# Optimization experiments

Measured on AMD Instinct MI355X. Metric: run time of the kernel, lower is better.

The kernel has to match this reference:

```python
import jax, jax.numpy as jnp
import numpy as np

N = 100_000        # nodes
E = 1_600_000      # edges
IN_F = 128         # input_features
HID = 64           # hiddens per head
OUT = 64           # outputs
NHEADS = 8
ALPHA = 0.2        # leaky_relu negative slope


def setup_inputs() -> dict:
    key = jax.random.key(0)
    ks = jax.random.split(key, 8)
    x = jax.random.normal(ks[0], (N, IN_F), jnp.float32)
    edges = jax.random.randint(ks[1], (2, E), 0, N)
    # nn.Linear(input_features, input_features)
    W0 = jax.random.normal(ks[2], (IN_F, IN_F), jnp.float32) / np.sqrt(IN_F).astype(np.float32)
    b0 = jnp.zeros((IN_F,), jnp.float32)
    # per-head SpGAT params: W [in, out], a [2*out]
    W_heads = jax.random.normal(ks[3], (NHEADS, IN_F, HID), jnp.float32) * 0.05
    a_heads = jax.random.normal(ks[4], (NHEADS, 2 * HID), jnp.float32) * 0.05
    W_end = jax.random.normal(ks[5], (NHEADS * HID, OUT), jnp.float32) * 0.05
    a_end = jax.random.normal(ks[6], (2 * OUT,), jnp.float32) * 0.05
    return dict(x=x, edges=edges, W0=W0, b0=b0,
                W_heads=W_heads, a_heads=a_heads, W_end=W_end, a_end=a_end)


def _sp_gat_layer(x, src, dst, W, a, apply_elu):
    """Standard sparse GAT layer (pyGAT SpGraphAttentionLayer).

    score_e = a . [h_src || h_dst];  e = exp(-leaky_relu(score))
    out_i = (sum_{e: src=i} e * h_dst) / (sum_{e: src=i} e)
    """
    n = x.shape[0]
    h = x @ W                      # [N, F]
    F = h.shape[1]
    # a.[h_i||h_j] decomposed into per-node scores to avoid [E, 2F] gather
    s_src = h @ a[:F]              # [N]
    s_dst = h @ a[F:]              # [N]
    score = s_src[src] + s_dst[dst]            # [E]
    edge_e = jnp.exp(-jax.nn.leaky_relu(score, ALPHA))
    rowsum = jax.ops.segment_sum(edge_e, src, num_segments=n)            # [N]
    agg = jax.ops.segment_sum(edge_e[:, None] * h[dst], src, num_segments=n)  # [N, F]
    out = agg / (rowsum[:, None] + 1e-16)
    return jax.nn.elu(out) if apply_elu else out


def reference(x, edges, W0, b0, W_heads, a_heads, W_end, a_end):
    src, dst = edges[0], edges[1]
    xp = x @ W0 + b0                                           # self.layer
    # multi-head attention, concat on feature dim (loop over fixed small head count)
    heads = [_sp_gat_layer(xp, src, dst, W_heads[i], a_heads[i], apply_elu=True)
             for i in range(NHEADS)]
    h = jnp.concatenate(heads, axis=1)                         # [N, NHEADS*HID]
    out = _sp_gat_layer(h, src, dst, W_end, a_end, apply_elu=False)  # [N, OUT]
    return jax.nn.softmax(out, axis=1)
```

## Files before the change

kernel.cpp:

```cpp
#include <hip/hip_runtime.h>


using bf16x8 = __bf16 __attribute__((ext_vector_type(8)));
using f32x4  = float  __attribute__((ext_vector_type(4)));

__device__ __forceinline__ unsigned short f2bf(float f) {
    __bf16 h = (__bf16)f;
    return __builtin_bit_cast(unsigned short, h);
}
__device__ __forceinline__ float bflo(unsigned int u) {
    return __builtin_bit_cast(float, u << 16);
}
__device__ __forceinline__ float bfhi(unsigned int u) {
    return __builtin_bit_cast(float, u & 0xffff0000u);
}
__device__ __forceinline__ float bfs(unsigned short u) {
    return __builtin_bit_cast(float, (unsigned)u << 16);
}
__device__ __forceinline__ int rdlane_i(int v, int l) {
    return __builtin_amdgcn_readlane(v, l);
}
__device__ __forceinline__ float rdlane_f(float v, int l) {
    return __builtin_bit_cast(float, __builtin_amdgcn_readlane(__builtin_bit_cast(int, v), l));
}
__device__ __forceinline__ float exp2fast(float x) {
#if __has_builtin(__builtin_amdgcn_exp2f)
    return __builtin_amdgcn_exp2f(x);
#else
    return exp2f(x);
#endif
}

#define ALPHA_NEG 0.2f
#define LOG2E 1.44269504088896340736f
#define CHUNK 20000
#define TILE 4096
#define VPT 16

__global__ void pack_all(const float* __restrict__ W0, const float* __restrict__ Wh,
                         const float* __restrict__ We, const float* __restrict__ ah,
                         unsigned short* __restrict__ W0t, unsigned short* __restrict__ Ballt,
                         unsigned short* __restrict__ Wendt, unsigned short* __restrict__ Bscore) {
    int b = blockIdx.x, t = threadIdx.x;
    if (b < 64) {
        int idx = b * 256 + t;
        int n = idx >> 7, k = idx & 127;
        W0t[n * 128 + k] = f2bf(W0[k * 128 + n]);
    } else if (b < 320) {
        int idx = (b - 64) * 256 + t;
        int c = idx >> 7, k = idx & 127;
        int h = c >> 6, f = c & 63;
        Ballt[idx] = f2bf(Wh[(h * 128 + k) * 64 + f]);
    } else if (b < 448) {
        int idx = (b - 320) * 256 + t;
        int n = idx >> 9, k = idx & 511;
        Wendt[idx] = f2bf(We[k * 64 + n]);
    } else {
        int idx = (b - 448) * 256 + t;
        if (idx < 1024) {
            int h = idx >> 7, k = idx & 127;
            float s = 0.f, d = 0.f;
            for (int f = 0; f < 64; f++) {
                float wv = Wh[(h * 128 + k) * 64 + f];
                s += wv * ah[h * 128 + f];
                d += wv * ah[h * 128 + 64 + f];
            }
            Bscore[h * 128 + k] = f2bf(s * LOG2E);
            Bscore[(8 + h) * 128 + k] = f2bf(d * LOG2E);
        }
    }
}

__global__ void csr_hist(const int* __restrict__ src, int* __restrict__ hb, int E) {
    __shared__ int h[512];
    int t = threadIdx.x, blk = blockIdx.x;
    h[t] = 0; h[t + 256] = 0;
    __syncthreads();
    int base = blk * TILE + t;
#pragma unroll
    for (int v = 0; v < VPT; v++) {
        int e = base + v * 256;
        if (e < E) atomicAdd(&h[src[e] >> 8], 1);
    }
    __syncthreads();
    hb[blk * 512 + t] = h[t];
    hb[blk * 512 + t + 256] = h[t + 256];
}

__global__ void csr_scan(int* __restrict__ hb, int* __restrict__ bkt_base, int ablk) {
    __shared__ int s[512];
    int t = threadIdx.x;
    int run = 0;
    for (int b0 = 0; b0 < ablk; b0 += 8) {
        int vv[8];
#pragma unroll
        for (int u = 0; u < 8; u++) {
            int blk = b0 + u;
            vv[u] = (blk < ablk) ? hb[blk * 512 + t] : 0;
        }
#pragma unroll
        for (int u = 0; u < 8; u++) {
            int blk = b0 + u;
            if (blk < ablk) hb[blk * 512 + t] = run;
            run += vv[u];
        }
    }
    s[t] = run;
    __syncthreads();
    for (int off = 1; off < 512; off <<= 1) {
        int add = (t >= off) ? s[t - off] : 0;
        __syncthreads();
        s[t] += add;
        __syncthreads();
    }
    bkt_base[t] = s[t] - run;
}

__global__ void csr_scatter(const int* __restrict__ src, const int* __restrict__ dst,
                            const int* __restrict__ hb, const int* __restrict__ bkt_base,
                            int2* __restrict__ pairs, int E) {
    __shared__ int cur[512];
    int t = threadIdx.x, blk = blockIdx.x;
    cur[t]       = hb[blk * 512 + t]       + bkt_base[t];
    cur[t + 256] = hb[blk * 512 + t + 256] + bkt_base[t + 256];
    __syncthreads();
    int base = blk * TILE + t;
#pragma unroll
    for (int v = 0; v < VPT; v++) {
        int e = base + v * 256;
        if (e < E) {
            int sv = src[e], dv = dst[e];
            int pos = atomicAdd(&cur[sv >> 8], 1);
            pairs[pos] = make_int2(sv, dv);
        }
    }
}

__global__ void csr_build(const int2* __restrict__ pairs, const int* __restrict__ bkt_base,
                          int* __restrict__ row_ptr, int* __restrict__ dstp, int n) {
    __shared__ int h[256];
    __shared__ int sc[256];
    int t = threadIdx.x, b = blockIdx.x;
    int e0 = bkt_base[b], e1 = bkt_base[b + 1];
    h[t] = 0;
    __syncthreads();
    for (int e = e0 + t; e < e1; e += 256) atomicAdd(&h[pairs[e].x & 255], 1);
    __syncthreads();
    int v = h[t];
    sc[t] = v;
    __syncthreads();
    for (int off = 1; off < 256; off <<= 1) {
        int add = (t >= off) ? sc[t - off] : 0;
        __syncthreads();
        sc[t] += add;
        __syncthreads();
    }
    int excl = sc[t] - v;
    int gid = (b << 8) + t;
    if (gid <= n) row_ptr[gid] = e0 + excl;
    h[t] = excl;
    __syncthreads();
    for (int e = e0 + t; e < e1; e += 256) {
        int2 pr = pairs[e];
        int pos = atomicAdd(&h[pr.x & 255], 1);
        dstp[e0 + pos] = pr.y;
    }
}

template <int BM, int BN, int K, int WM, int WN, int MT, int NT,
          bool AF32, bool BIAS, bool OBF16, bool ELU, bool BATCHZ>
__launch_bounds__(256)
__global__ void gemm_mfma(const void* __restrict__ Ap, const unsigned short* __restrict__ Bt,
                          const float* __restrict__ bias, void* __restrict__ Cp, int M,
                          int lda, int ldc) {
    constexpr int LDK = 40;
    __shared__ unsigned short As[BM * LDK];
    __shared__ unsigned short Bs[BN * LDK];
    const int t = threadIdx.x;
    const long m0 = (long)blockIdx.x * BM;
    const long n0 = (long)blockIdx.y * BN;
    const int abase = BATCHZ ? blockIdx.z * K : 0;
    const unsigned short* Btz = BATCHZ ? Bt + (size_t)blockIdx.z * BN * K : Bt;
    const long cbase = BATCHZ ? (long)blockIdx.z * BN : 0;
    const int wave = t >> 6, lane = t & 63;
    const int wm = wave / WN, wn = wave % WN;
    const int lrow = lane & 15, lq = lane >> 4;

    f32x4 acc[MT][NT];
#pragma unroll
    for (int a = 0; a < MT; a++)
#pragma unroll
        for (int b = 0; b < NT; b++) acc[a][b] = (f32x4)0.0f;

    for (int kt = 0; kt < K / 32; kt++) {
        const int k0 = kt * 32;
        if constexpr (AF32) {
            const float* A = (const float*)Ap;
#pragma unroll
            for (int it = 0; it < BM * 8 / 256; it++) {
                int L = t + 256 * it;
                int row = L >> 3, kc = (L & 7) * 4;
                long gr = m0 + row;
                float4 v = make_float4(0.f, 0.f, 0.f, 0.f);
                if (gr < M) v = *(const float4*)&A[gr * lda + abase + k0 + kc];
                unsigned int lo = (unsigned)f2bf(v.x) | ((unsigned)f2bf(v.y) << 16);
                unsigned int hi = (unsigned)f2bf(v.z) | ((unsigned)f2bf(v.w) << 16);
                *(uint2*)&As[row * LDK + kc] = make_uint2(lo, hi);
            }
        } else {
            const unsigned short* A = (const unsigned short*)Ap;
#pragma unroll
            for (int it = 0; it < BM * 4 / 256; it++) {
                int L = t + 256 * it;
                int row = L >> 2, kc = (L & 3) * 8;
                long gr = m0 + row;
                uint4 v = make_uint4(0u, 0u, 0u, 0u);
                if (gr < M) v = *(const uint4*)&A[gr * lda + abase + k0 + kc];
                *(uint4*)&As[row * LDK + kc] = v;
            }
        }
#pragma unroll
        for (int it = 0; it < (BN * 4 + 255) / 256; it++) {
            int L = t + 256 * it;
            if (L < BN * 4) {
                int row = L >> 2, kc = (L & 3) * 8;
                *(uint4*)&Bs[row * LDK + kc] = *(const uint4*)&Btz[(n0 + row) * K + k0 + kc];
            }
        }
        __syncthreads();

        bf16x8 af[MT], bfr[NT];
#pragma unroll
        for (int mt = 0; mt < MT; mt++)
            af[mt] = *(const bf16x8*)&As[((wm * MT + mt) * 16 + lrow) * LDK + lq * 8];
#pragma unroll
        for (int nt = 0; nt < NT; nt++)
            bfr[nt] = *(const bf16x8*)&Bs[((wn * NT + nt) * 16 + lrow) * LDK + lq * 8];
#pragma unroll
        for (int mt = 0; mt < MT; mt++)
#pragma unroll
            for (int nt = 0; nt < NT; nt++)
                acc[mt][nt] = __builtin_amdgcn_mfma_f32_16x16x32_bf16(af[mt], bfr[nt],
                                                                     acc[mt][nt], 0, 0, 0);
        __syncthreads();
    }

#pragma unroll
    for (int mt = 0; mt < MT; mt++) {
        long rbase = m0 + (wm * MT + mt) * 16 + lq * 4;
#pragma unroll
        for (int nt = 0; nt < NT; nt++) {
            long col = cbase + n0 + (wn * NT + nt) * 16 + lrow;
            float bv = 0.f;
            if constexpr (BIAS) bv = bias[col];
#pragma unroll
            for (int r = 0; r < 4; r++) {
                long row = rbase + r;
                if (row < M) {
                    float v = acc[mt][nt][r] + bv;
                    if constexpr (ELU) v = v > 0.f ? v : __expf(v) - 1.0f;
                    if constexpr (OBF16)
                        ((unsigned short*)Cp)[row * ldc + col] = f2bf(v);
                    else
                        ((float*)Cp)[row * ldc + col] = v;
                }
            }
        }
    }
}

__global__ void agg_xp(const int* __restrict__ row_ptr, const int* __restrict__ dstp,
                       const float* __restrict__ s16,
                       const unsigned short* __restrict__ xp, unsigned short* __restrict__ z,
                       int n0, int n1) {
    int t = threadIdx.x, wave = t >> 6, lane = t & 63;
    int i = n0 + blockIdx.x * 4 + wave;
    if (i >= n1) return;
    int e0 = __builtin_amdgcn_readfirstlane(row_ptr[i]);
    int e1 = __builtin_amdgcn_readfirstlane(row_ptr[i + 1]);
    const int hl = lane & 7, sub8 = lane >> 3;
    const int voff = lane << 1;
    float ssv = s16[(size_t)i * 16 + hl];
    float acc[16];
#pragma unroll
    for (int c = 0; c < 16; c++) acc[c] = 0.f;
    float rsl = 0.f;

    for (int p = e0; p < e1; p += 8) {
        int idx = p + sub8;
        int cl = idx < e1 ? idx : e1 - 1;
        int jv = dstp[cl];
        float sc = s16[(size_t)(unsigned)jv * 16 + 8 + hl];
        float s = ssv + sc;
        s = fmaxf(s, ALPHA_NEG * s);
        float wv = (idx < e1) ? exp2fast(-s) : 0.f;
        rsl += wv;
        int nem = e1 - p;
        unsigned xv[8];
#pragma unroll
        for (int u = 0; u < 8; u++) {
            if (u < nem) {
                int ju = rdlane_i(jv, u * 8);
                xv[u] = *(const unsigned*)&xp[(size_t)(unsigned)ju * 128 + voff];
            }
        }
#pragma unroll
        for (int u = 0; u < 8; u++) {
            if (u < nem) {
                float lo = bflo(xv[u]), hi = bfhi(xv[u]);
#pragma unroll
                for (int h = 0; h < 8; h++) {
                    float wh = rdlane_f(wv, u * 8 + h);
                    acc[2 * h]     += wh * lo;
                    acc[2 * h + 1] += wh * hi;
                }
            }
        }
    }

    rsl += __shfl_xor(rsl, 8, 64);
    rsl += __shfl_xor(rsl, 16, 64);
    rsl += __shfl_xor(rsl, 32, 64);
    float inv = 1.0f / (rsl + 1e-16f);
    size_t zb = (size_t)(i - n0) * 1024 + voff;
#pragma unroll
    for (int h = 0; h < 8; h++) {
        float ih = rdlane_f(inv, h);
        unsigned pw = (unsigned)f2bf(acc[2 * h] * ih) |
                      ((unsigned)f2bf(acc[2 * h + 1] * ih) << 16);
        *(unsigned*)&z[zb + h * 128] = pw;
    }
}

__global__ void scores2(const unsigned short* __restrict__ h2b, const float* __restrict__ ae,
                        float* __restrict__ ss2, float* __restrict__ sd2, int n) {
    int t = threadIdx.x, wave = t >> 6, lane = t & 63;
    int i = blockIdx.x * 4 + wave;
    if (i >= n) return;
    float v = bfs(h2b[(size_t)i * 64 + lane]);
    float a = v * ae[lane];
    float b = v * ae[64 + lane];
    for (int d = 32; d > 0; d >>= 1) {
        a += __shfl_xor(a, d, 64);
        b += __shfl_xor(b, d, 64);
    }
    if (lane == 0) { ss2[i] = a * LOG2E; sd2[i] = b * LOG2E; }
}

__global__ void agg_final(const int* __restrict__ row_ptr, const int* __restrict__ dstp,
                          const float* __restrict__ ss2, const float* __restrict__ sd2,
                          const unsigned short* __restrict__ h2b, float* __restrict__ out,
                          int n) {
    int t = threadIdx.x, wave = t >> 6, lane = t & 63;
    int i = blockIdx.x * 4 + wave;
    if (i >= n) return;
    int e0 = __builtin_amdgcn_readfirstlane(row_ptr[i]);
    int e1 = __builtin_amdgcn_readfirstlane(row_ptr[i + 1]);
    float ssrc = ss2[i];
    float acc = 0.f, rsl = 0.f;
    for (int base = e0; base < e1; base += 64) {
        int cnt = e1 - base; if (cnt > 64) cnt = 64;
        int jv = 0; float wv = 0.f;
        if (lane < cnt) {
            jv = dstp[base + lane];
            float sc = ssrc + sd2[jv];
            sc = fmaxf(sc, ALPHA_NEG * sc);
            wv = exp2fast(-sc);
        }
        rsl += wv;
        int q = 0;
        for (; q + 8 <= cnt; q += 8) {
            float vv[8], ww[8];
#pragma unroll
            for (int u = 0; u < 8; u++) {
                int j = rdlane_i(jv, q + u);
                vv[u] = bfs(h2b[((size_t)(unsigned)j << 6) + lane]);
                ww[u] = rdlane_f(wv, q + u);
            }
#pragma unroll
            for (int u = 0; u < 8; u++) acc += ww[u] * vv[u];
        }
        for (; q < cnt; q++) {
            int j = rdlane_i(jv, q);
            float w = rdlane_f(wv, q);
            acc += w * bfs(h2b[((size_t)(unsigned)j << 6) + lane]);
        }
    }
    float rs = rsl;
    for (int d = 32; d > 0; d >>= 1) rs += __shfl_xor(rs, d, 64);
    float o = acc / (rs + 1e-16f);
    float m = o;
    for (int d = 32; d > 0; d >>= 1) m = fmaxf(m, __shfl_xor(m, d, 64));
    float e = __expf(o - m);
    float s = e;
    for (int d = 32; d > 0; d >>= 1) s += __shfl_xor(s, d, 64);
    out[(size_t)i * 64 + lane] = e / s;
}

extern "C" void kernel_launch(void* const* d_in, const int* in_sizes, int n_in,
                              void* d_out, int out_size, void* d_ws, size_t ws_size,
                              hipStream_t stream) {
    const float* x  = (const float*)d_in[0];
    const int* edges = (const int*)d_in[1];
    const float* W0 = (const float*)d_in[2];
    const float* b0 = (const float*)d_in[3];
    const float* Wh = (const float*)d_in[4];
    const float* ah = (const float*)d_in[5];
    const float* We = (const float*)d_in[6];
    const float* ae = (const float*)d_in[7];
    float* dout = (float*)d_out;

    const int Nn = in_sizes[0] / 128;
    const int E  = in_sizes[1] / 2;
    const int* src = edges;
    const int* dst = edges + E;

    char* p = (char*)d_ws;
    auto alloc = [&](size_t bytes) -> char* {
        char* r = p;
        p += (bytes + 255) & ~(size_t)255;
        return r;
    };
    unsigned short* W0t   = (unsigned short*)alloc(128 * 128 * 2);
    unsigned short* Ballt = (unsigned short*)alloc(512 * 128 * 2);
    unsigned short* Wendt = (unsigned short*)alloc((size_t)64 * 512 * 2);
    unsigned short* Bscore = (unsigned short*)alloc(16 * 128 * 2);
    const int ablk = (E + TILE - 1) / TILE;
    int* hist_blk = (int*)alloc((size_t)ablk * 512 * 4);
    int* bkt_base = (int*)alloc(512 * 4);
    int* row_ptr = (int*)alloc((size_t)(Nn + 1) * 4);
    int* dstp    = (int*)alloc((size_t)E * 4);
    float* s16   = (float*)alloc((size_t)Nn * 16 * 4);
    float* ss2   = (float*)alloc((size_t)Nn * 4);
    float* sd2   = (float*)alloc((size_t)Nn * 4);
    unsigned short* xp = (unsigned short*)alloc((size_t)Nn * 128 * 2);
    unsigned short* z  = (unsigned short*)alloc((size_t)CHUNK * 1024 * 2);
    unsigned short* hcat = (unsigned short*)alloc((size_t)Nn * 512 * 2);
    unsigned short* h2b = (unsigned short*)z;
    int2* pairs = (int2*)hcat;

    size_t needed = (size_t)(p - (char*)d_ws);
    if (needed > ws_size) return;

    const int gm = (Nn + 127) / 128;
    const int nbkt = (Nn + 255) >> 8;

    pack_all<<<452, 256, 0, stream>>>(W0, Wh, We, ah, W0t, Ballt, Wendt, Bscore);

    csr_hist<<<ablk, 256, 0, stream>>>(src, hist_blk, E);
    csr_scan<<<1, 512, 0, stream>>>(hist_blk, bkt_base, ablk);
    csr_scatter<<<ablk, 256, 0, stream>>>(src, dst, hist_blk, bkt_base, pairs, E);
    csr_build<<<nbkt, 256, 0, stream>>>(pairs, bkt_base, row_ptr, dstp, Nn);

    gemm_mfma<128, 128, 128, 2, 2, 4, 4, true, true, true, false, false>
        <<<dim3(gm, 1), 256, 0, stream>>>(x, W0t, b0, xp, Nn, 128, 128);

    gemm_mfma<128, 16, 128, 4, 1, 2, 1, false, false, false, false, false>
        <<<dim3(gm, 1), 256, 0, stream>>>(xp, Bscore, nullptr, s16, Nn, 128, 16);

    for (int c0 = 0; c0 < Nn; c0 += CHUNK) {
        int c1 = min(c0 + CHUNK, Nn);
        int Mc = c1 - c0;
        agg_xp<<<(Mc + 3) / 4, 256, 0, stream>>>(row_ptr, dstp, s16, xp, z, c0, c1);
        gemm_mfma<128, 64, 128, 4, 1, 2, 4, false, false, true, true, true>
            <<<dim3((Mc + 127) / 128, 1, 8), 256, 0, stream>>>(
                z, Ballt, nullptr, hcat + (size_t)c0 * 512, Mc, 1024, 512);
    }

    gemm_mfma<128, 64, 512, 4, 1, 2, 4, false, false, true, false, false>
        <<<dim3(gm, 1), 256, 0, stream>>>(hcat, Wendt, nullptr, h2b, Nn, 512, 64);

    scores2<<<(Nn + 3) / 4, 256, 0, stream>>>(h2b, ae, ss2, sd2, Nn);
    agg_final<<<(Nn + 3) / 4, 256, 0, stream>>>(row_ptr, dstp, ss2, sd2, h2b, dout, Nn);
}
```

Measured before the change: 560.3 us.

## Precompute edge attention weights in separate passes before aggregation

Splits edge-weight computation out of both aggregation kernels into new wpass1/wpass2 kernels that write per-edge exp weights and per-node inverse row sums to global buffers. The aggregation kernels then read the weights with vector loads and use readfirstlane on dst indices instead of cross-lane readlane broadcasts. This is meant to cut the per-edge scalar/readlane overhead in the inner loops. The cost is extra launches and roughly 51MB of weight writes plus rereads (E*8 floats), and w2 aliases the hcat buffer after it has been consumed.

Measured after the change: 670.5 us. 1.2x slower.

```diff
diff --git a/kernel.cpp b/kernel.cpp
--- a/kernel.cpp
+++ b/kernel.cpp
@@ -17,11 +17,8 @@
 __device__ __forceinline__ float bfs(unsigned short u) {
     return __builtin_bit_cast(float, (unsigned)u << 16);
 }
-__device__ __forceinline__ int rdlane_i(int v, int l) {
-    return __builtin_amdgcn_readlane(v, l);
-}
-__device__ __forceinline__ float rdlane_f(float v, int l) {
-    return __builtin_bit_cast(float, __builtin_amdgcn_readlane(__builtin_bit_cast(int, v), l));
+__device__ __forceinline__ int rfl(int v) {
+    return __builtin_amdgcn_readfirstlane(v);
 }
 __device__ __forceinline__ float exp2fast(float x) {
 #if __has_builtin(__builtin_amdgcn_exp2f)
@@ -269,23 +266,17 @@
     }
 }
 
-__global__ void agg_xp(const int* __restrict__ row_ptr, const int* __restrict__ dstp,
-                       const float* __restrict__ s16,
-                       const unsigned short* __restrict__ xp, unsigned short* __restrict__ z,
-                       int n0, int n1) {
+__global__ void wpass1(const int* __restrict__ row_ptr, const int* __restrict__ dstp,
+                       const float* __restrict__ s16, float* __restrict__ w8,
+                       float* __restrict__ inv8, int n) {
     int t = threadIdx.x, wave = t >> 6, lane = t & 63;
-    int i = n0 + blockIdx.x * 4 + wave;
-    if (i >= n1) return;
-    int e0 = __builtin_amdgcn_readfirstlane(row_ptr[i]);
-    int e1 = __builtin_amdgcn_readfirstlane(row_ptr[i + 1]);
+    int i = blockIdx.x * 4 + wave;
+    if (i >= n) return;
+    int e0 = rfl(row_ptr[i]);
+    int e1 = rfl(row_ptr[i + 1]);
     const int hl = lane & 7, sub8 = lane >> 3;
-    const int voff = lane << 1;
     float ssv = s16[(size_t)i * 16 + hl];
-    float acc[16];
-#pragma unroll
-    for (int c = 0; c < 16; c++) acc[c] = 0.f;
     float rsl = 0.f;
-
     for (int p = e0; p < e1; p += 8) {
         int idx = p + sub8;
         int cl = idx < e1 ? idx : e1 - 1;
@@ -295,39 +286,65 @@
         s = fmaxf(s, ALPHA_NEG * s);
         float wv = (idx < e1) ? exp2fast(-s) : 0.f;
         rsl += wv;
-        int nem = e1 - p;
-        unsigned xv[8];
-#pragma unroll
-        for (int u = 0; u < 8; u++) {
-            if (u < nem) {
-                int ju = rdlane_i(jv, u * 8);
-                xv[u] = *(const unsigned*)&xp[(size_t)(unsigned)ju * 128 + voff];
-            }
-        }
-#pragma unroll
-        for (int u = 0; u < 8; u++) {
-            if (u < nem) {
-                float lo = bflo(xv[u]), hi = bfhi(xv[u]);
-#pragma unroll
-                for (int h = 0; h < 8; h++) {
-                    float wh = rdlane_f(wv, u * 8 + h);
-                    acc[2 * h]     += wh * lo;
-                    acc[2 * h + 1] += wh * hi;
-                }
-            }
-        }
-    }
-
+        if (idx < e1) w8[(size_t)idx * 8 + hl] = wv;
+    }
     rsl += __shfl_xor(rsl, 8, 64);
     rsl += __shfl_xor(rsl, 16, 64);
     rsl += __shfl_xor(rsl, 32, 64);
     float inv = 1.0f / (rsl + 1e-16f);
+    if (lane < 8) inv8[(size_t)i * 8 + lane] = inv;
+}
+
+__global__ void agg_xp(const int* __restrict__ row_ptr, const int* __restrict__ dstp,
+                       const float* __restrict__ w8, const float* __restrict__ inv8,
+                       const unsigned short* __restrict__ xp, unsigned short* __restrict__ z,
+                       int n0, int n1) {
+    int t = threadIdx.x, wave = t >> 6, lane = t & 63;
+    int i = n0 + blockIdx.x * 4 + wave;
+    if (i >= n1) return;
+    int e0 = rfl(row_ptr[i]);
+    int e1 = rfl(row_ptr[i + 1]);
+    const int voff = lane << 1;
+    float acc[16];
+#pragma unroll
+    for (int c = 0; c < 16; c++) acc[c] = 0.f;
+
+    for (int p = e0; p < e1; p += 8) {
+        int nem = e1 - p;
+        unsigned xv[8];
+#pragma unroll
+        for (int u = 0; u < 8; u++) {
+            if (u < nem) {
+                int ju = rfl(dstp[p + u]);
+                xv[u] = *(const unsigned*)&xp[(size_t)(unsigned)ju * 128 + voff];
+            }
+        }
+#pragma unroll
+        for (int u = 0; u < 8; u++) {
+            if (u < nem) {
+                const float4 wa = *(const float4*)&w8[(size_t)(p + u) * 8];
+                const float4 wb = *(const float4*)&w8[(size_t)(p + u) * 8 + 4];
+                float lo = bflo(xv[u]), hi = bfhi(xv[u]);
+                acc[0]  += wa.x * lo; acc[1]  += wa.x * hi;
+                acc[2]  += wa.y * lo; acc[3]  += wa.y * hi;
+                acc[4]  += wa.z * lo; acc[5]  += wa.z * hi;
+                acc[6]  += wa.w * lo; acc[7]  += wa.w * hi;
+                acc[8]  += wb.x * lo; acc[9]  += wb.x * hi;
+                acc[10] += wb.y * lo; acc[11] += wb.y * hi;
+                acc[12] += wb.z * lo; acc[13] += wb.z * hi;
+                acc[14] += wb.w * lo; acc[15] += wb.w * hi;
+            }
+        }
+    }
+
+    const float4 ia = *(const float4*)&inv8[(size_t)i * 8];
+    const float4 ib = *(const float4*)&inv8[(size_t)i * 8 + 4];
+    const float iv[8] = {ia.x, ia.y, ia.z, ia.w, ib.x, ib.y, ib.z, ib.w};
     size_t zb = (size_t)(i - n0) * 1024 + voff;
 #pragma unroll
     for (int h = 0; h < 8; h++) {
-        float ih = rdlane_f(inv, h);
-        unsigned pw = (unsigned)f2bf(acc[2 * h] * ih) |
-                      ((unsigned)f2bf(acc[2 * h + 1] * ih) << 16);
+        unsigned pw = (unsigned)f2bf(acc[2 * h] * iv[h]) |
+                      ((unsigned)f2bf(acc[2 * h + 1] * iv[h]) << 16);
         *(unsigned*)&z[zb + h * 128] = pw;
     }
 }
@@ -347,48 +364,56 @@
     if (lane == 0) { ss2[i] = a * LOG2E; sd2[i] = b * LOG2E; }
 }
 
+__global__ void wpass2(const int* __restrict__ row_ptr, const int* __restrict__ dstp,
+                       const float* __restrict__ ss2, const float* __restrict__ sd2,
+                       float* __restrict__ w2, float* __restrict__ inv2, int n) {
+    int t = threadIdx.x, wave = t >> 6, lane = t & 63;
+    int i = blockIdx.x * 4 + wave;
+    if (i >= n) return;
+    int e0 = rfl(row_ptr[i]);
+    int e1 = rfl(row_ptr[i + 1]);
+    float ssrc = ss2[i];
+    float rsl = 0.f;
+    for (int base = e0; base < e1; base += 64) {
+        int idx = base + lane;
+        int cl = idx < e1 ? idx : e1 - 1;
+        int j = dstp[cl];
+        float sc = ssrc + sd2[j];
+        sc = fmaxf(sc, ALPHA_NEG * sc);
+        float wv = (idx < e1) ? exp2fast(-sc) : 0.f;
+        rsl += wv;
+        if (idx < e1) w2[idx] = wv;
+    }
+    for (int d = 32; d > 0; d >>= 1) rsl += __shfl_xor(rsl, d, 64);
+    if (lane == 0) inv2[i] = 1.0f / (rsl + 1e-16f);
+}
+
 __global__ void agg_final(const int* __restrict__ row_ptr, const int* __restrict__ dstp,
-                          const float* __restrict__ ss2, const float* __restrict__ sd2,
+                          const float* __restrict__ w2, const float* __restrict__ inv2,
                           const unsigned short* __restrict__ h2b, float* __restrict__ out,
                           int n) {
     int t = threadIdx.x, wave = t >> 6, lane = t & 63;
     int i = blockIdx.x * 4 + wave;
     if (i >= n) return;
-    int e0 = __builtin_amdgcn_readfirstlane(row_ptr[i]);
-    int e1 = __builtin_amdgcn_readfirstlane(row_ptr[i + 1]);
-    float ssrc = ss2[i];
-    float acc = 0.f, rsl = 0.f;
-    for (int base = e0; base < e1; base += 64) {
-        int cnt = e1 - base; if (cnt > 64) cnt = 64;
-        int jv = 0; float wv = 0.f;
-        if (lane < cnt) {
-            jv = dstp[base + lane];
-            float sc = ssrc + sd2[jv];
-            sc = fmaxf(sc, ALPHA_NEG * sc);
-            wv = exp2fast(-sc);
-        }
-        rsl += wv;
-        int q = 0;
-        for (; q + 8 <= cnt; q += 8) {
-            float vv[8], ww[8];
-#pragma unroll
-            for (int u = 0; u < 8; u++) {
-                int j = rdlane_i(jv, q + u);
+    int e0 = rfl(row_ptr[i]);
+    int e1 = rfl(row_ptr[i + 1]);
+    float acc = 0.f;
+    for (int p = e0; p < e1; p += 8) {
+        int nem = e1 - p;
+        float vv[8], ww[8];
+#pragma unroll
+        for (int u = 0; u < 8; u++) {
+            if (u < nem) {
+                int j = rfl(dstp[p + u]);
                 vv[u] = bfs(h2b[((size_t)(unsigned)j << 6) + lane]);
-                ww[u] = rdlane_f(wv, q + u);
-            }
-#pragma unroll
-            for (int u = 0; u < 8; u++) acc += ww[u] * vv[u];
-        }
-        for (; q < cnt; q++) {
-            int j = rdlane_i(jv, q);
-            float w = rdlane_f(wv, q);
-            acc += w * bfs(h2b[((size_t)(unsigned)j << 6) + lane]);
-        }
-    }
-    float rs = rsl;
-    for (int d = 32; d > 0; d >>= 1) rs += __shfl_xor(rs, d, 64);
-    float o = acc / (rs + 1e-16f);
+                ww[u] = w2[p + u];
+            }
+        }
+#pragma unroll
+        for (int u = 0; u < 8; u++)
+            if (u < nem) acc += ww[u] * vv[u];
+    }
+    float o = acc * inv2[i];
     float m = o;
     for (int d = 32; d > 0; d >>= 1) m = fmaxf(m, __shfl_xor(m, d, 64));
     float e = __expf(o - m);
@@ -433,11 +458,15 @@
     float* s16   = (float*)alloc((size_t)Nn * 16 * 4);
     float* ss2   = (float*)alloc((size_t)Nn * 4);
     float* sd2   = (float*)alloc((size_t)Nn * 4);
+    float* w8    = (float*)alloc((size_t)E * 8 * 4);
+    float* inv8  = (float*)alloc((size_t)Nn * 8 * 4);
+    float* inv2  = (float*)alloc((size_t)Nn * 4);
     unsigned short* xp = (unsigned short*)alloc((size_t)Nn * 128 * 2);
     unsigned short* z  = (unsigned short*)alloc((size_t)CHUNK * 1024 * 2);
     unsigned short* hcat = (unsigned short*)alloc((size_t)Nn * 512 * 2);
     unsigned short* h2b = (unsigned short*)z;
     int2* pairs = (int2*)hcat;
+    float* w2 = (float*)hcat;
 
     size_t needed = (size_t)(p - (char*)d_ws);
     if (needed > ws_size) return;
@@ -458,10 +487,12 @@
     gemm_mfma<128, 16, 128, 4, 1, 2, 1, false, false, false, false, false>
         <<<dim3(gm, 1), 256, 0, stream>>>(xp, Bscore, nullptr, s16, Nn, 128, 16);
 
+    wpass1<<<(Nn + 3) / 4, 256, 0, stream>>>(row_ptr, dstp, s16, w8, inv8, Nn);
+
     for (int c0 = 0; c0 < Nn; c0 += CHUNK) {
         int c1 = min(c0 + CHUNK, Nn);
         int Mc = c1 - c0;
-        agg_xp<<<(Mc + 3) / 4, 256, 0, stream>>>(row_ptr, dstp, s16, xp, z, c0, c1);
+        agg_xp<<<(Mc + 3) / 4, 256, 0, stream>>>(row_ptr, dstp, w8, inv8, xp, z, c0, c1);
         gemm_mfma<128, 64, 128, 4, 1, 2, 4, false, false, true, true, true>
             <<<dim3((Mc + 127) / 128, 1, 8), 256, 0, stream>>>(
                 z, Ballt, nullptr, hcat + (size_t)c0 * 512, Mc, 1024, 512);
@@ -471,5 +502,6 @@
         <<<dim3(gm, 1), 256, 0, stream>>>(hcat, Wendt, nullptr, h2b, Nn, 512, 64);
 
     scores2<<<(Nn + 3) / 4, 256, 0, stream>>>(h2b, ae, ss2, sd2, Nn);
-    agg_final<<<(Nn + 3) / 4, 256, 0, stream>>>(row_ptr, dstp, ss2, sd2, h2b, dout, Nn);
-}
+    wpass2<<<(Nn + 3) / 4, 256, 0, stream>>>(row_ptr, dstp, ss2, sd2, w2, inv2, Nn);
+    agg_final<<<(Nn + 3) / 4, 256, 0, stream>>>(row_ptr, dstp, w2, inv2, h2b, dout, Nn);
+}
```
